# Performance work log

Measured on AMD Instinct MI355X. Metric: run time of the kernel, lower is better.

Reference implementation:

```python
import jax, jax.numpy as jnp
import numpy as np

WORD, D, H = 512, 64, 8  # word_size, embed_dim (per-head), n_query

def setup_inputs() -> dict:
    key = jax.random.key(0)
    ks = jax.random.split(key, 9)
    B, S = 2, 4096
    sw = 1.0 / np.sqrt(WORD)
    x  = jax.random.normal(ks[0], (B, S, WORD), dtype=jnp.float32)
    Wk = jax.random.normal(ks[1], (WORD, D), dtype=jnp.float32) * sw
    bk = jnp.zeros((D,), jnp.float32)
    Wv = jax.random.normal(ks[2], (WORD, D), dtype=jnp.float32) * sw
    bv = jnp.zeros((D,), jnp.float32)
    Wq = jax.random.normal(ks[3], (H, WORD, D), dtype=jnp.float32) * sw
    bq = jnp.zeros((H, D), jnp.float32)
    Wp = jax.random.normal(ks[4], (H * D, D), dtype=jnp.float32) * (1.0 / np.sqrt(H * D))
    bp = jnp.zeros((D,), jnp.float32)
    return {"x": x, "Wq": Wq, "bq": bq, "Wk": Wk, "bk": bk, "Wv": Wv, "bv": bv, "Wp": Wp, "bp": bp}

def reference(x, Wq, bq, Wk, bk, Wv, bv, Wp, bp):
    # shared K/V across all query heads (multi-query attention)
    K = x @ Wk + bk                                   # [b, s, d]
    V = x @ Wv + bv                                   # [b, s, d]
    Q = jnp.einsum('bsw,hwd->bhsd', x, Wq) + bq[None, :, None, :]  # [b, h, s, d]
    scale = 1.0 / jnp.sqrt(jnp.float32(D))
    scores = jnp.einsum('bhsd,btd->bhst', Q, K) * scale  # [b, h, s, t]
    attn = jax.nn.softmax(scores, axis=-1)
    Z = jnp.einsum('bhst,btd->bhsd', attn, V)            # [b, h, s, d]
    B, _, S, _ = Z.shape
    Zc = jnp.transpose(Z, (0, 2, 1, 3)).reshape(B, S, H * D)  # concat heads
    return Zc @ Wp + bp                                   # [b, s, d]
```

## Files before the change

kernel.cpp:

```cpp
#include <hip/hip_runtime.h>
#include <hip/hip_bf16.h>
#include <stdint.h>

#define BB 2
#define SS 4096
#define WW 512
#define DD 64
#define HH 8
#define QSCALE 0.1803368801111244f

typedef __hip_bfloat16 bf16;
typedef __bf16 bf16x8 __attribute__((ext_vector_type(8)));
typedef float f32x16 __attribute__((ext_vector_type(16)));
typedef unsigned int u32x4 __attribute__((ext_vector_type(4)));
typedef unsigned int u32x2 __attribute__((ext_vector_type(2)));

union U4 { u32x4 u4; unsigned int u[4]; bf16x8 v; };

__device__ __forceinline__ float ldv(const float* p, size_t i) { return p[i]; }
__device__ __forceinline__ float ldv(const bf16* p, size_t i)  { return __bfloat162float(p[i]); }

__device__ __forceinline__ unsigned short f2bu(float f) {
    union Ub { bf16 b; unsigned short u; } t;
    t.b = __float2bfloat16(f);
    return t.u;
}

__device__ __forceinline__ float fast_exp2(float x) {
#if __has_builtin(__builtin_amdgcn_exp2f)
    return __builtin_amdgcn_exp2f(x);
#else
    return exp2f(x);
#endif
}

__device__ __forceinline__ f32x16 mfma_bf16(bf16x8 a, bf16x8 b, f32x16 c) {
    return __builtin_amdgcn_mfma_f32_32x32x16_bf16(a, b, c, 0, 0, 0);
}

__device__ __forceinline__ unsigned int pk_bf16(float lo, float hi) {
    unsigned int a = __float_as_uint(lo) + 0x8000u;
    unsigned int b = __float_as_uint(hi) + 0x8000u;
    return __builtin_amdgcn_perm(b, a, 0x07060302u);
}

__device__ __forceinline__ unsigned int cvtpk_bf16(float lo, float hi) {
    unsigned int r;
    asm("v_cvt_pk_bf16_f32 %0, %1, %2" : "=v"(r) : "v"(lo), "v"(hi));
    return r;
}

__device__ __forceinline__ int block_detect(const void* raw, int* cntLds)
{
    if (threadIdx.x == 0) *cntLds = 0;
    __syncthreads();
    const bf16* xb = (const bf16*)raw;
    const float v = __bfloat162float(xb[2 * threadIdx.x]);
    const float a = fabsf(v);
    const bool insane = !(v == v) || (a >= 1.0e4f) || (a != 0.0f && a <= 1.0e-8f);
    const unsigned long long m = __ballot(insane);
    if ((threadIdx.x & 63) == 0) atomicAdd(cntLds, __popcll(m));
    __syncthreads();
    return (*cntLds * 2 > 256) ? 1 : 0;
}

template<typename T>
__device__ __forceinline__ void prep_w_body(
    const T* Wq, const T* bq, const T* Wk, const T* bk,
    const T* Wv, const T* bv, const T* Wp, const T* bp,
    unsigned short* Wb, float* bb, float (*Tt)[65], int pwblk)
{
    const int tid = threadIdx.x;
    const int cg = pwblk >> 3, wg = pwblk & 7;
    const int c0 = cg * 64, w0 = wg * 64;
    const T* src = (cg == 0) ? Wk : (cg == 1) ? Wv
                 : (cg == 10) ? Wp : (Wq + (size_t)(cg - 2) * WW * DD);
    const float scale = (cg >= 2 && cg < 10) ? QSCALE : 1.0f;

    #pragma unroll
    for (int i = 0; i < 16; ++i) {
        const int e = i * 256 + tid, w = e >> 6, d = e & 63;
        Tt[w][d] = ldv(src, (size_t)(w0 + w) * DD + d) * scale;
    }
    __syncthreads();
    #pragma unroll
    for (int i = 0; i < 16; ++i) {
        const int e = i * 256 + tid, d = e >> 6, w = e & 63;
        Wb[(size_t)(c0 + d) * WW + w0 + w] = f2bu(Tt[w][d]);
    }
    if (pwblk == 0) {
        #pragma unroll
        for (int i = 0; i < 3; ++i) {
            const int c = tid + i * 256;
            if (c < 704) {
                float v;
                if (c < 64)       v = ldv(bk, c);
                else if (c < 128) v = ldv(bv, c - 64);
                else if (c < 640) v = ldv(bq, c - 128) * QSCALE;
                else              v = ldv(bp, c - 640);
                bb[c] = v;
            }
        }
    }
}

__global__ __launch_bounds__(256) void prep_kernel(
    const void* x, const void* Wq, const void* bq, const void* Wk, const void* bk,
    const void* Wv, const void* bv, const void* Wp, const void* bp,
    unsigned short* xb, unsigned short* Wb, float* bb, int* flag)
{
    __shared__ float Tt[64][65];
    __shared__ int cnt;
    const int blk = blockIdx.x;

    if (blk < 2048) {
        const int fl = block_detect(x, &cnt);
        if (blk == 0 && threadIdx.x == 0) *flag = fl;
        const size_t i = ((size_t)blk * 256 + threadIdx.x) * 8;
        if (fl) {
            const float4* p = (const float4*)((const float*)x + i);
            const float4 a = p[0], b = p[1];
            unsigned int w[4];
            w[0] = pk_bf16(a.x, a.y); w[1] = pk_bf16(a.z, a.w);
            w[2] = pk_bf16(b.x, b.y); w[3] = pk_bf16(b.z, b.w);
            *(u32x4*)(xb + i) = *(u32x4*)w;
        } else {
            *(u32x4*)(xb + i) = *(const u32x4*)((const unsigned short*)x + i);
        }
    } else {
        const int fl = block_detect(Wk, &cnt);
        if (fl)
            prep_w_body<float>((const float*)Wq, (const float*)bq, (const float*)Wk,
                               (const float*)bk, (const float*)Wv, (const float*)bv,
                               (const float*)Wp, (const float*)bp, Wb, bb, Tt, blk - 2048);
        else
            prep_w_body<bf16>((const bf16*)Wq, (const bf16*)bq, (const bf16*)Wk,
                              (const bf16*)bk, (const bf16*)Wv, (const bf16*)bv,
                              (const bf16*)Wp, (const bf16*)bp, Wb, bb, Tt, blk - 2048);
    }
}

#define KP 40

__global__ __launch_bounds__(256, 2) void proj_mfma_kernel(
    const unsigned short* __restrict__ xb, const unsigned short* __restrict__ Wb,
    const float* __restrict__ bb,
    bf16* __restrict__ Kb, bf16* __restrict__ Vb, bf16* __restrict__ Qb)
{
    __shared__ unsigned short As[2][128 * KP];
    __shared__ unsigned short Bs[2][128 * KP];

    const int tid = threadIdx.x;
    const int wv = tid >> 6, ln = tid & 63;
    const int g = ln >> 5, cc = ln & 31;
    const int nblk = blockIdx.x % 5, mblk = blockIdx.x / 5;
    const int row0 = mblk * 128, n0 = nblk * 128;
    const int wm = (wv & 1) * 64, wn = (wv >> 1) * 64;

    const int sm = tid >> 2;
    const int sko = (tid & 3) * 8;

    u32x4 pa[2], pb[2];
    #define GLOAD(kt)                                                          \
        do {                                                                   \
            _Pragma("unroll")                                                  \
            for (int i = 0; i < 2; ++i) {                                      \
                const int m = sm + i * 64;                                     \
                pa[i] = *(const u32x4*)&xb[(size_t)(row0 + m) * WW + (kt) * 32 + sko]; \
                pb[i] = *(const u32x4*)&Wb[(size_t)(n0 + m) * WW + (kt) * 32 + sko];   \
            }                                                                  \
        } while (0)
    #define LWRITE(buf)                                                        \
        do {                                                                   \
            _Pragma("unroll")                                                  \
            for (int i = 0; i < 2; ++i) {                                      \
                const int m = sm + i * 64;                                     \
                *(u32x4*)&As[buf][m * KP + sko] = pa[i];                       \
                *(u32x4*)&Bs[buf][m * KP + sko] = pb[i];                       \
            }                                                                  \
        } while (0)

    f32x16 acc[2][2];
    #pragma unroll
    for (int a = 0; a < 2; ++a)
        #pragma unroll
        for (int c2 = 0; c2 < 2; ++c2)
            #pragma unroll
            for (int i = 0; i < 16; ++i) acc[a][c2][i] = 0.f;

    GLOAD(0); LWRITE(0);
    GLOAD(1);

    for (int kt = 0; kt < 16; ++kt) {
        __syncthreads();
        const int buf = kt & 1;
        #pragma unroll
        for (int ks = 0; ks < 2; ++ks) {
            U4 af[2], bfr[2];
            #pragma unroll
            for (int ms = 0; ms < 2; ++ms)
                af[ms].u4 = *(const u32x4*)&As[buf][(wm + ms * 32 + cc) * KP + ks * 16 + g * 8];
            #pragma unroll
            for (int ns = 0; ns < 2; ++ns)
                bfr[ns].u4 = *(const u32x4*)&Bs[buf][(wn + ns * 32 + cc) * KP + ks * 16 + g * 8];
            #pragma unroll
            for (int ms = 0; ms < 2; ++ms)
                #pragma unroll
                for (int ns = 0; ns < 2; ++ns)
                    acc[ms][ns] = mfma_bf16(af[ms].v, bfr[ns].v, acc[ms][ns]);
        }
        if (kt < 15) {
            LWRITE(buf ^ 1);
            if (kt < 14) GLOAD(kt + 2);
        }
    }
    #undef GLOAD
    #undef LWRITE

    const int b = row0 >> 12;
    #pragma unroll
    for (int ns = 0; ns < 2; ++ns) {
        const int c = n0 + wn + ns * 32 + cc;
        const int grp = c >> 6, d = c & 63;
        const float bias = bb[c];
        bf16* base = (grp == 0) ? Kb : (grp == 1) ? Vb
                   : Qb + (size_t)((b * HH + grp - 2) - b) * SS * DD;
        #pragma unroll
        for (int ms = 0; ms < 2; ++ms) {
            #pragma unroll
            for (int reg = 0; reg < 16; ++reg) {
                const int r = (reg & 3) + 8 * (reg >> 2) + 4 * g;
                const int row = row0 + wm + ms * 32 + r;
                base[(size_t)row * DD + d] = __float2bfloat16(acc[ms][ns][reg] + bias);
            }
        }
    }
}

__device__ __forceinline__ int vperm(int r) {
    return (r & ~31) + 16 * ((r >> 4) & 1) + 8 * ((r >> 2) & 1)
         + 4 * ((r >> 3) & 1) + (r & 3);
}

__global__ __launch_bounds__(256) void vtrans_kernel(
    const unsigned short* __restrict__ Vb, unsigned short* __restrict__ Vtg)
{
    __shared__ unsigned short Ls[64 * 70];
    const int tid = threadIdx.x;
    const int bb = blockIdx.x >> 6;
    const int t0 = (blockIdx.x & 63) * 64;
    const unsigned short* in = Vb + ((size_t)bb * SS + t0) * DD;

    const int lt = tid >> 2, s2 = tid & 3;
    #pragma unroll
    for (int q2 = 0; q2 < 2; ++q2) {
        const int sg = s2 + q2 * 4;
        *(u32x4*)&Ls[lt * 70 + sg * 8] = *(const u32x4*)&in[lt * 64 + sg * 8];
    }
    __syncthreads();

    const int dd = tid >> 2, t2 = tid & 3;
    unsigned short* op = Vtg + ((size_t)bb * DD + dd) * SS + t0;
    #pragma unroll
    for (int q2 = 0; q2 < 2; ++q2) {
        const int ts = (t2 + q2 * 4) * 8;
        unsigned short tmp[8];
        #pragma unroll
        for (int j = 0; j < 8; ++j) tmp[j] = Ls[(ts + j) * 70 + dd];
        const int s0 = vperm(ts);
        const int s1 = vperm(ts + 4);
        *(u32x2*)&op[s0] = *(u32x2*)&tmp[0];
        *(u32x2*)&op[s1] = *(u32x2*)&tmp[4];
    }
}

#define VTP 72
#define ZP_PART ((size_t)16 * 64 * 4096)
#define LP_PART ((size_t)16 * 4096)

template<int TSPLIT>
__global__ __launch_bounds__(256, 2) void attn_mfma_kernel(
    const bf16* __restrict__ Kb, const unsigned short* __restrict__ Vtg,
    const bf16* __restrict__ Qb, bf16* __restrict__ Zb,
    float* __restrict__ Zp, float* __restrict__ Lp)
{
    __shared__ unsigned short Vt[2][64 * VTP];
    __shared__ unsigned short Kt[2][64 * VTP];

    const int tid = threadIdx.x;
    const int wv = tid >> 6, ln = tid & 63;
    const int g  = ln >> 5, cc = ln & 31;
    constexpr int TSB = (TSPLIT == 1) ? 0 : (TSPLIT == 2) ? 1 : 2;
    const int chunk = blockIdx.x & 15;
    const int tsp = (blockIdx.x >> 4) & (TSPLIT - 1);
    const int bh  = blockIdx.x >> (4 + TSB);
    const int b = bh >> 3, h = bh & 7;
    const int qw = chunk * 256 + wv * 64;
    const int it0 = tsp * (64 / TSPLIT);
    const int itN = it0 + 64 / TSPLIT;

    const unsigned short* Kg = (const unsigned short*)(Kb + (size_t)b * SS * DD);
    const unsigned short* Vg = Vtg + (size_t)b * DD * SS;
    const char* Qg = (const char*)(Qb + (size_t)(b * HH + h) * SS * DD);

    const int sr = tid >> 2, sc = (tid & 3) * 16;
    const unsigned short* VgRow = Vg + (size_t)sr * SS;

    U4 qf[2][4];
    #pragma unroll
    for (int nt = 0; nt < 2; ++nt)
        #pragma unroll
        for (int ks = 0; ks < 4; ++ks)
            qf[nt][ks].u4 = *(const u32x4*)(Qg +
                (size_t)((qw + nt * 32 + cc) * 64 + g * 8 + ks * 16) * 2);

    const f32x16 fzero = {0.f, 0.f, 0.f, 0.f, 0.f, 0.f, 0.f, 0.f,
                          0.f, 0.f, 0.f, 0.f, 0.f, 0.f, 0.f, 0.f};
    U4 ones;
    ones.u[0] = 0x3F803F80u; ones.u[1] = 0x3F803F80u;
    ones.u[2] = 0x3F803F80u; ones.u[3] = 0x3F803F80u;

    f32x16 zacc[2][2];
    #pragma unroll
    for (int nt = 0; nt < 2; ++nt)
        #pragma unroll
        for (int dt = 0; dt < 2; ++dt)
            #pragma unroll
            for (int i = 0; i < 16; ++i) zacc[nt][dt][i] = 0.f;

    f32x16 lacc[2];
    #pragma unroll
    for (int nt = 0; nt < 2; ++nt)
        #pragma unroll
        for (int i = 0; i < 16; ++i) lacc[nt][i] = 0.f;

    {
        const unsigned short* ksrc = Kg + (size_t)(it0 * 64 + sr) * 64 + sc;
        const unsigned short* vsrc = VgRow + it0 * 64 + sc;
        *(u32x4*)&Kt[0][sr * VTP + sc + 0] = *(const u32x4*)&ksrc[0];
        *(u32x4*)&Kt[0][sr * VTP + sc + 8] = *(const u32x4*)&ksrc[8];
        *(u32x4*)&Vt[0][sr * VTP + sc + 0] = *(const u32x4*)&vsrc[0];
        *(u32x4*)&Vt[0][sr * VTP + sc + 8] = *(const u32x4*)&vsrc[8];
    }

    for (int it = it0; it < itN; ++it) {
        __syncthreads();
        const int buf = it & 1;
        const bool more = (it + 1) < itN;
        u32x4 pk0, pk1, pv0, pv1;
        if (more) {
            const unsigned short* ksrc = Kg + (size_t)((it + 1) * 64 + sr) * 64 + sc;
            const unsigned short* vsrc = VgRow + (it + 1) * 64 + sc;
            pk0 = *(const u32x4*)&ksrc[0];
            pk1 = *(const u32x4*)&ksrc[8];
            pv0 = *(const u32x4*)&vsrc[0];
            pv1 = *(const u32x4*)&vsrc[8];
        }

        #pragma unroll
        for (int si = 0; si < 2; ++si) {
            U4 kf[4];
            #pragma unroll
            for (int ks = 0; ks < 4; ++ks)
                kf[ks].u4 = *(const u32x4*)&Kt[buf][(si * 32 + cc) * VTP +
                                                    ks * 16 + g * 8];
            U4 vf[2][2];
            #pragma unroll
            for (int ks = 0; ks < 2; ++ks)
                #pragma unroll
                for (int dt = 0; dt < 2; ++dt)
                    vf[ks][dt].u4 = *(const u32x4*)&Vt[buf][(dt * 32 + cc) * VTP +
                                                            si * 32 + ks * 16 + g * 8];

            #pragma unroll
            for (int nt = 0; nt < 2; ++nt) {
                __builtin_amdgcn_s_setprio(1);
                f32x16 s = mfma_bf16(kf[0].v, qf[nt][0].v, fzero);
                #pragma unroll
                for (int ks = 1; ks < 4; ++ks) s = mfma_bf16(kf[ks].v, qf[nt][ks].v, s);
                __builtin_amdgcn_s_setprio(0);

                float p[16];
                #pragma unroll
                for (int i = 0; i < 16; ++i) p[i] = fast_exp2(s[i]);
                unsigned int w0[8];
                #pragma unroll
                for (int i2 = 0; i2 < 8; ++i2)
                    w0[i2] = cvtpk_bf16(p[2 * i2], p[2 * i2 + 1]);

                __builtin_amdgcn_s_setprio(1);
                #pragma unroll
                for (int ks = 0; ks < 2; ++ks) {
                    U4 pb;
                    pb.u[0] = w0[ks * 4 + 0]; pb.u[1] = w0[ks * 4 + 1];
                    pb.u[2] = w0[ks * 4 + 2]; pb.u[3] = w0[ks * 4 + 3];
                    lacc[nt] = mfma_bf16(ones.v, pb.v, lacc[nt]);
                    #pragma unroll
                    for (int dt = 0; dt < 2; ++dt)
                        zacc[nt][dt] = mfma_bf16(vf[ks][dt].v, pb.v, zacc[nt][dt]);
                }
                __builtin_amdgcn_s_setprio(0);
            }
        }

        if (more) {
            *(u32x4*)&Kt[buf ^ 1][sr * VTP + sc + 0] = pk0;
            *(u32x4*)&Kt[buf ^ 1][sr * VTP + sc + 8] = pk1;
            *(u32x4*)&Vt[buf ^ 1][sr * VTP + sc + 0] = pv0;
            *(u32x4*)&Vt[buf ^ 1][sr * VTP + sc + 8] = pv1;
        }
    }

    float l[2];
    l[0] = lacc[0][0];
    l[1] = lacc[1][0];

    if (TSPLIT == 1) {
        #pragma unroll
        for (int nt = 0; nt < 2; ++nt) {
            const float rr = 1.0f / l[nt];
            bf16* zp = Zb + (size_t)(b * SS + qw + nt * 32 + cc) * (HH * DD)
                     + h * DD + g * 4;
            #pragma unroll
            for (int dt = 0; dt < 2; ++dt)
                #pragma unroll
                for (int i = 0; i < 16; ++i) {
                    const int d = (i & 3) + 8 * (i >> 2) + 32 * dt;
                    zp[d] = __float2bfloat16(zacc[nt][dt][i] * rr);
                }
        }
    } else {
        float* zp0 = Zp + (size_t)(tsp * 16 + bh) * (64 * 4096);
        #pragma unroll
        for (int nt = 0; nt < 2; ++nt) {
            const int q = qw + nt * 32 + cc;
            #pragma unroll
            for (int dt = 0; dt < 2; ++dt)
                #pragma unroll
                for (int i = 0; i < 16; ++i) {
                    const int d = (i & 3) + 8 * (i >> 2) + 4 * g + 32 * dt;
                    zp0[(size_t)d * 4096 + q] = zacc[nt][dt][i];
                }
            if (g == 0)
                Lp[(size_t)(tsp * 16 + bh) * 4096 + q] = l[nt];
        }
    }
}

template<int NP>
__global__ __launch_bounds__(256) void combine_kernel(
    const float* __restrict__ Zp, const float* __restrict__ Lp,
    bf16* __restrict__ Zb)
{
    const size_t T = (size_t)blockIdx.x * 256 + threadIdx.x;
    const int sblk = (int)(T & 511);
    const int d  = (int)((T >> 9) & 63);
    const int bh = (int)(T >> 15);
    const int s0 = sblk * 8;
    const int b = bh >> 3, h = bh & 7;

    const float* p0 = Zp + ((size_t)bh * 64 + d) * 4096 + s0;
    const float* l0 = Lp + (size_t)bh * 4096 + s0;

    float z[8], lv[8];
    #pragma unroll
    for (int j = 0; j < 8; ++j) { z[j] = 0.f; lv[j] = 0.f; }
    #pragma unroll
    for (int np = 0; np < NP; ++np) {
        const float* p = p0 + (size_t)np * ZP_PART;
        const float* l = l0 + (size_t)np * LP_PART;
        #pragma unroll
        for (int j = 0; j < 8; j += 4) {
            const float4 a = *(const float4*)(p + j);
            z[j] += a.x; z[j+1] += a.y; z[j+2] += a.z; z[j+3] += a.w;
            const float4 e = *(const float4*)(l + j);
            lv[j] += e.x; lv[j+1] += e.y; lv[j+2] += e.z; lv[j+3] += e.w;
        }
    }
    bf16* zo = Zb + ((size_t)(b * SS + s0)) * (HH * DD) + h * DD + d;
    #pragma unroll
    for (int j = 0; j < 8; ++j)
        zo[(size_t)j * (HH * DD)] = __float2bfloat16(z[j] / lv[j]);
}

__global__ __launch_bounds__(256) void outp_mfma_kernel(
    const bf16* __restrict__ Zb, const unsigned short* __restrict__ Wb,
    const float* __restrict__ bb, const int* flag, void* out)
{
    __shared__ unsigned short As[2][128 * KP];
    __shared__ unsigned short Bs[2][64 * KP];

    const int tid = threadIdx.x;
    const int wv = tid >> 6, ln = tid & 63;
    const int g = ln >> 5, cc = ln & 31;
    const int row0 = blockIdx.x * 128;
    const int sm = tid >> 2, sko = (tid & 3) * 8;

    const unsigned short* Zu = (const unsigned short*)Zb;
    const unsigned short* Wn = Wb + (size_t)640 * WW;
    const float* bbp = bb + 640;

    u32x4 pa[2], pbv;
    #define GLOAD2(kt)                                                         \
        do {                                                                   \
            _Pragma("unroll")                                                  \
            for (int i = 0; i < 2; ++i)                                        \
                pa[i] = *(const u32x4*)&Zu[(size_t)(row0 + sm + i * 64) * WW + (kt) * 32 + sko]; \
            pbv = *(const u32x4*)&Wn[(size_t)sm * WW + (kt) * 32 + sko];       \
        } while (0)
    #define LWRITE2(buf)                                                       \
        do {                                                                   \
            _Pragma("unroll")                                                  \
            for (int i = 0; i < 2; ++i)                                        \
                *(u32x4*)&As[buf][(sm + i * 64) * KP + sko] = pa[i];           \
            *(u32x4*)&Bs[buf][sm * KP + sko] = pbv;                            \
        } while (0)

    f32x16 acc[2];
    #pragma unroll
    for (int ns = 0; ns < 2; ++ns)
        #pragma unroll
        for (int i = 0; i < 16; ++i) acc[ns][i] = 0.f;

    GLOAD2(0); LWRITE2(0);
    GLOAD2(1);

    for (int kt = 0; kt < 16; ++kt) {
        __syncthreads();
        const int buf = kt & 1;
        #pragma unroll
        for (int ks = 0; ks < 2; ++ks) {
            U4 af;
            af.u4 = *(const u32x4*)&As[buf][(wv * 32 + cc) * KP + ks * 16 + g * 8];
            #pragma unroll
            for (int ns = 0; ns < 2; ++ns) {
                U4 bf2;
                bf2.u4 = *(const u32x4*)&Bs[buf][(ns * 32 + cc) * KP + ks * 16 + g * 8];
                acc[ns] = mfma_bf16(af.v, bf2.v, acc[ns]);
            }
        }
        if (kt < 15) {
            LWRITE2(buf ^ 1);
            if (kt < 14) GLOAD2(kt + 2);
        }
    }
    #undef GLOAD2
    #undef LWRITE2

    const int fl = *flag;
    #pragma unroll
    for (int ns = 0; ns < 2; ++ns) {
        const int c = ns * 32 + cc;
        const float bias = bbp[c];
        #pragma unroll
        for (int reg = 0; reg < 16; ++reg) {
            const int r = (reg & 3) + 8 * (reg >> 2) + 4 * g;
            const int row = row0 + wv * 32 + r;
            const float v = acc[ns][reg] + bias;
            if (fl) ((float*)out)[(size_t)row * DD + c] = v;
            else    ((bf16*)out)[(size_t)row * DD + c] = __float2bfloat16(v);
        }
    }
}

extern "C" void kernel_launch(void* const* d_in, const int* in_sizes, int n_in,
                              void* d_out, int out_size, void* d_ws, size_t ws_size,
                              hipStream_t stream)
{
    const void* x  = d_in[0];
    const void* Wq = d_in[1];
    const void* bq = d_in[2];
    const void* Wk = d_in[3];
    const void* bk = d_in[4];
    const void* Wv = d_in[5];
    const void* bv = d_in[6];
    const void* Wp = d_in[7];
    const void* bp = d_in[8];

    char* ws = (char*)d_ws;
    bf16* Kb = (bf16*)(ws);
    bf16* Vb = (bf16*)(ws + (1u << 20));
    bf16* Qb = (bf16*)(ws + (2u << 20));
    bf16* Zb = (bf16*)(ws + (10u << 20));
    unsigned short* xb = (unsigned short*)(ws + (10u << 20));
    int* flag = (int*)(ws + (18u << 20));
    unsigned short* Wb = (unsigned short*)(ws + (18u << 20) + 64);
    float* bb = (float*)(ws + (18u << 20) + 64 + 704 * 512 * 2);
    unsigned short* Vtg = (unsigned short*)(ws + (19u << 20));
    float* Zp = (float*)(ws + (20u << 20));

    const size_t ws_need2 = (20u << 20) + (size_t)2 * ZP_PART * 4 + (size_t)2 * LP_PART * 4;

    prep_kernel<<<2136, 256, 0, stream>>>(x, Wq, bq, Wk, bk, Wv, bv, Wp, bp,
                                          xb, Wb, bb, flag);
    proj_mfma_kernel<<<320, 256, 0, stream>>>(xb, Wb, bb, Kb, Vb, Qb);
    vtrans_kernel<<<128, 256, 0, stream>>>((const unsigned short*)Vb, Vtg);
    if (ws_size >= ws_need2) {
        float* Lp = (float*)(ws + (20u << 20) + 2 * ZP_PART * 4);
        attn_mfma_kernel<2><<<512, 256, 0, stream>>>(Kb, Vtg, Qb, Zb, Zp, Lp);
        combine_kernel<2><<<2048, 256, 0, stream>>>(Zp, Lp, Zb);
    } else {
        float* Lp = (float*)(ws + (20u << 20));
        attn_mfma_kernel<1><<<256, 256, 0, stream>>>(Kb, Vtg, Qb, Zb, Zp, Lp);
    }
    outp_mfma_kernel<<<64, 256, 0, stream>>>(Zb, Wb, bb, flag, d_out);
}
```

Measured before the change: 201.7 us.

## Halve per-warp query tile in attention to double block count

Each wave now handles 32 queries instead of 64, so a block covers 128 queries and the attention grid doubles to 1024 (or 512 without split) blocks. This cuts per-thread register use (one Q fragment set and one set of accumulators) and spreads work across more CUs. In exchange, every K/V tile loaded into shared memory is reused by half as many queries, which doubles global and LDS traffic for K/V.

```diff
diff --git a/kernel.cpp b/kernel.cpp
--- a/kernel.cpp
+++ b/kernel.cpp
@@ -291,11 +291,11 @@
     const int wv = tid >> 6, ln = tid & 63;
     const int g  = ln >> 5, cc = ln & 31;
     constexpr int TSB = (TSPLIT == 1) ? 0 : (TSPLIT == 2) ? 1 : 2;
-    const int chunk = blockIdx.x & 15;
-    const int tsp = (blockIdx.x >> 4) & (TSPLIT - 1);
-    const int bh  = blockIdx.x >> (4 + TSB);
+    const int chunk = blockIdx.x & 31;
+    const int tsp = (blockIdx.x >> 5) & (TSPLIT - 1);
+    const int bh  = blockIdx.x >> (5 + TSB);
     const int b = bh >> 3, h = bh & 7;
-    const int qw = chunk * 256 + wv * 64;
+    const int qw = chunk * 128 + wv * 32;
     const int it0 = tsp * (64 / TSPLIT);
     const int itN = it0 + 64 / TSPLIT;
 
@@ -306,13 +306,11 @@
     const int sr = tid >> 2, sc = (tid & 3) * 16;
     const unsigned short* VgRow = Vg + (size_t)sr * SS;
 
-    U4 qf[2][4];
-    #pragma unroll
-    for (int nt = 0; nt < 2; ++nt)
-        #pragma unroll
-        for (int ks = 0; ks < 4; ++ks)
-            qf[nt][ks].u4 = *(const u32x4*)(Qg +
-                (size_t)((qw + nt * 32 + cc) * 64 + g * 8 + ks * 16) * 2);
+    U4 qf[4];
+    #pragma unroll
+    for (int ks = 0; ks < 4; ++ks)
+        qf[ks].u4 = *(const u32x4*)(Qg +
+            (size_t)((qw + cc) * 64 + g * 8 + ks * 16) * 2);
 
     const f32x16 fzero = {0.f, 0.f, 0.f, 0.f, 0.f, 0.f, 0.f, 0.f,
                           0.f, 0.f, 0.f, 0.f, 0.f, 0.f, 0.f, 0.f};
@@ -320,19 +318,15 @@
     ones.u[0] = 0x3F803F80u; ones.u[1] = 0x3F803F80u;
     ones.u[2] = 0x3F803F80u; ones.u[3] = 0x3F803F80u;
 
-    f32x16 zacc[2][2];
-    #pragma unroll
-    for (int nt = 0; nt < 2; ++nt)
-        #pragma unroll
-        for (int dt = 0; dt < 2; ++dt)
-            #pragma unroll
-            for (int i = 0; i < 16; ++i) zacc[nt][dt][i] = 0.f;
-
-    f32x16 lacc[2];
-    #pragma unroll
-    for (int nt = 0; nt < 2; ++nt)
-        #pragma unroll
-        for (int i = 0; i < 16; ++i) lacc[nt][i] = 0.f;
+    f32x16 zacc[2];
+    #pragma unroll
+    for (int dt = 0; dt < 2; ++dt)
+        #pragma unroll
+        for (int i = 0; i < 16; ++i) zacc[dt][i] = 0.f;
+
+    f32x16 lacc;
+    #pragma unroll
+    for (int i = 0; i < 16; ++i) lacc[i] = 0.f;
 
     {
         const unsigned short* ksrc = Kg + (size_t)(it0 * 64 + sr) * 64 + sc;
@@ -372,35 +366,32 @@
                     vf[ks][dt].u4 = *(const u32x4*)&Vt[buf][(dt * 32 + cc) * VTP +
                                                             si * 32 + ks * 16 + g * 8];
 
-            #pragma unroll
-            for (int nt = 0; nt < 2; ++nt) {
-                __builtin_amdgcn_s_setprio(1);
-                f32x16 s = mfma_bf16(kf[0].v, qf[nt][0].v, fzero);
+            __builtin_amdgcn_s_setprio(1);
+            f32x16 s = mfma_bf16(kf[0].v, qf[0].v, fzero);
+            #pragma unroll
+            for (int ks = 1; ks < 4; ++ks) s = mfma_bf16(kf[ks].v, qf[ks].v, s);
+            __builtin_amdgcn_s_setprio(0);
+
+            float p[16];
+            #pragma unroll
+            for (int i = 0; i < 16; ++i) p[i] = fast_exp2(s[i]);
+            unsigned int w0[8];
+            #pragma unroll
+            for (int i2 = 0; i2 < 8; ++i2)
+                w0[i2] = cvtpk_bf16(p[2 * i2], p[2 * i2 + 1]);
+
+            __builtin_amdgcn_s_setprio(1);
+            #pragma unroll
+            for (int ks = 0; ks < 2; ++ks) {
+                U4 pb;
+                pb.u[0] = w0[ks * 4 + 0]; pb.u[1] = w0[ks * 4 + 1];
+                pb.u[2] = w0[ks * 4 + 2]; pb.u[3] = w0[ks * 4 + 3];
+                lacc = mfma_bf16(ones.v, pb.v, lacc);
                 #pragma unroll
-                for (int ks = 1; ks < 4; ++ks) s = mfma_bf16(kf[ks].v, qf[nt][ks].v, s);
-                __builtin_amdgcn_s_setprio(0);
-
-                float p[16];
-                #pragma unroll
-                for (int i = 0; i < 16; ++i) p[i] = fast_exp2(s[i]);
-                unsigned int w0[8];
-                #pragma unroll
-                for (int i2 = 0; i2 < 8; ++i2)
-                    w0[i2] = cvtpk_bf16(p[2 * i2], p[2 * i2 + 1]);
-
-                __builtin_amdgcn_s_setprio(1);
-                #pragma unroll
-                for (int ks = 0; ks < 2; ++ks) {
-                    U4 pb;
-                    pb.u[0] = w0[ks * 4 + 0]; pb.u[1] = w0[ks * 4 + 1];
-                    pb.u[2] = w0[ks * 4 + 2]; pb.u[3] = w0[ks * 4 + 3];
-                    lacc[nt] = mfma_bf16(ones.v, pb.v, lacc[nt]);
-                    #pragma unroll
-                    for (int dt = 0; dt < 2; ++dt)
-                        zacc[nt][dt] = mfma_bf16(vf[ks][dt].v, pb.v, zacc[nt][dt]);
-                }
-                __builtin_amdgcn_s_setprio(0);
+                for (int dt = 0; dt < 2; ++dt)
+                    zacc[dt] = mfma_bf16(vf[ks][dt].v, pb.v, zacc[dt]);
             }
+            __builtin_amdgcn_s_setprio(0);
         }
 
         if (more) {
@@ -411,39 +402,30 @@
         }
     }
 
-    float l[2];
-    l[0] = lacc[0][0];
-    l[1] = lacc[1][0];
+    const float l = lacc[0];
 
     if (TSPLIT == 1) {
-        #pragma unroll
-        for (int nt = 0; nt < 2; ++nt) {
-            const float rr = 1.0f / l[nt];
-            bf16* zp = Zb + (size_t)(b * SS + qw + nt * 32 + cc) * (HH * DD)
-                     + h * DD + g * 4;
-            #pragma unroll
-            for (int dt = 0; dt < 2; ++dt)
-                #pragma unroll
-                for (int i = 0; i < 16; ++i) {
-                    const int d = (i & 3) + 8 * (i >> 2) + 32 * dt;
-                    zp[d] = __float2bfloat16(zacc[nt][dt][i] * rr);
-                }
-        }
+        const float rr = 1.0f / l;
+        bf16* zp = Zb + (size_t)(b * SS + qw + cc) * (HH * DD) + h * DD + g * 4;
+        #pragma unroll
+        for (int dt = 0; dt < 2; ++dt)
+            #pragma unroll
+            for (int i = 0; i < 16; ++i) {
+                const int d = (i & 3) + 8 * (i >> 2) + 32 * dt;
+                zp[d] = __float2bfloat16(zacc[dt][i] * rr);
+            }
     } else {
         float* zp0 = Zp + (size_t)(tsp * 16 + bh) * (64 * 4096);
-        #pragma unroll
-        for (int nt = 0; nt < 2; ++nt) {
-            const int q = qw + nt * 32 + cc;
-            #pragma unroll
-            for (int dt = 0; dt < 2; ++dt)
-                #pragma unroll
-                for (int i = 0; i < 16; ++i) {
-                    const int d = (i & 3) + 8 * (i >> 2) + 4 * g + 32 * dt;
-                    zp0[(size_t)d * 4096 + q] = zacc[nt][dt][i];
-                }
-            if (g == 0)
-                Lp[(size_t)(tsp * 16 + bh) * 4096 + q] = l[nt];
-        }
+        const int q = qw + cc;
+        #pragma unroll
+        for (int dt = 0; dt < 2; ++dt)
+            #pragma unroll
+            for (int i = 0; i < 16; ++i) {
+                const int d = (i & 3) + 8 * (i >> 2) + 4 * g + 32 * dt;
+                zp0[(size_t)d * 4096 + q] = zacc[dt][i];
+            }
+        if (g == 0)
+            Lp[(size_t)(tsp * 16 + bh) * 4096 + q] = l;
     }
 }
 
@@ -597,11 +579,11 @@
     vtrans_kernel<<<128, 256, 0, stream>>>((const unsigned short*)Vb, Vtg);
     if (ws_size >= ws_need2) {
         float* Lp = (float*)(ws + (20u << 20) + 2 * ZP_PART * 4);
-        attn_mfma_kernel<2><<<512, 256, 0, stream>>>(Kb, Vtg, Qb, Zb, Zp, Lp);
+        attn_mfma_kernel<2><<<1024, 256, 0, stream>>>(Kb, Vtg, Qb, Zb, Zp, Lp);
         combine_kernel<2><<<2048, 256, 0, stream>>>(Zp, Lp, Zb);
     } else {
         float* Lp = (float*)(ws + (20u << 20));
-        attn_mfma_kernel<1><<<256, 256, 0, stream>>>(Kb, Vtg, Qb, Zb, Zp, Lp);
+        attn_mfma_kernel<1><<<512, 256, 0, stream>>>(Kb, Vtg, Qb, Zb, Zp, Lp);
     }
     outp_mfma_kernel<<<64, 256, 0, stream>>>(Zb, Wb, bb, flag, d_out);
 }
```

Measured after the change: 209.1 us. 3.7% more time.

## Fuse V transpose into projection epilogue and split-K combine into attention

Applied to the files above, without the earlier changes.

The projection kernel now writes V directly in the transposed, permuted layout the attention kernel expects, which removes the separate vtrans kernel and the Vb round trip. The attention kernel with a two-way key split now uses a per-tile atomic counter, so whichever block of a pair finishes second reads the partner's partial Z and L, normalises, and writes Zb. This removes the separate combine kernel and its launch. In exchange the V stores become scattered 2-byte writes, and correctness depends on threadfence ordering and on cflags being reset in prep_kernel on every call.

```diff
diff --git a/kernel.cpp b/kernel.cpp
--- a/kernel.cpp
+++ b/kernel.cpp
@@ -107,7 +107,7 @@
 __global__ __launch_bounds__(256) void prep_kernel(
     const void* x, const void* Wq, const void* bq, const void* Wk, const void* bk,
     const void* Wv, const void* bv, const void* Wp, const void* bp,
-    unsigned short* xb, unsigned short* Wb, float* bb, int* flag)
+    unsigned short* xb, unsigned short* Wb, float* bb, int* flag, int* cflags)
 {
     __shared__ float Tt[64][65];
     __shared__ int cnt;
@@ -128,6 +128,7 @@
             *(u32x4*)(xb + i) = *(const u32x4*)((const unsigned short*)x + i);
         }
     } else {
+        if (blk == 2048) cflags[threadIdx.x] = 0;
         const int fl = block_detect(Wk, &cnt);
         if (fl)
             prep_w_body<float>((const float*)Wq, (const float*)bq, (const float*)Wk,
@@ -145,7 +146,7 @@
 __global__ __launch_bounds__(256, 2) void proj_mfma_kernel(
     const unsigned short* __restrict__ xb, const unsigned short* __restrict__ Wb,
     const float* __restrict__ bb,
-    bf16* __restrict__ Kb, bf16* __restrict__ Vb, bf16* __restrict__ Qb)
+    bf16* __restrict__ Kb, unsigned short* __restrict__ Vtg, bf16* __restrict__ Qb)
 {
     __shared__ unsigned short As[2][128 * KP];
     __shared__ unsigned short Bs[2][128 * KP];
@@ -223,54 +224,31 @@
         const int c = n0 + wn + ns * 32 + cc;
         const int grp = c >> 6, d = c & 63;
         const float bias = bb[c];
-        bf16* base = (grp == 0) ? Kb : (grp == 1) ? Vb
-                   : Qb + (size_t)((b * HH + grp - 2) - b) * SS * DD;
-        #pragma unroll
-        for (int ms = 0; ms < 2; ++ms) {
-            #pragma unroll
-            for (int reg = 0; reg < 16; ++reg) {
-                const int r = (reg & 3) + 8 * (reg >> 2) + 4 * g;
-                const int row = row0 + wm + ms * 32 + r;
-                base[(size_t)row * DD + d] = __float2bfloat16(acc[ms][ns][reg] + bias);
+        if (grp == 1) {
+            unsigned short* vt = Vtg + ((size_t)(b * DD + d)) * SS;
+            #pragma unroll
+            for (int ms = 0; ms < 2; ++ms) {
+                #pragma unroll
+                for (int reg = 0; reg < 16; ++reg) {
+                    const int r = (reg & 3) + 8 * (reg >> 2) + 4 * g;
+                    const int lrow = (row0 & 4095) + wm + ms * 32 + r;
+                    const int srow = (lrow & ~12) | ((lrow & 4) << 1) | ((lrow & 8) >> 1);
+                    vt[srow] = f2bu(acc[ms][ns][reg] + bias);
+                }
             }
-        }
-    }
-}
-
-__device__ __forceinline__ int vperm(int r) {
-    return (r & ~31) + 16 * ((r >> 4) & 1) + 8 * ((r >> 2) & 1)
-         + 4 * ((r >> 3) & 1) + (r & 3);
-}
-
-__global__ __launch_bounds__(256) void vtrans_kernel(
-    const unsigned short* __restrict__ Vb, unsigned short* __restrict__ Vtg)
-{
-    __shared__ unsigned short Ls[64 * 70];
-    const int tid = threadIdx.x;
-    const int bb = blockIdx.x >> 6;
-    const int t0 = (blockIdx.x & 63) * 64;
-    const unsigned short* in = Vb + ((size_t)bb * SS + t0) * DD;
-
-    const int lt = tid >> 2, s2 = tid & 3;
-    #pragma unroll
-    for (int q2 = 0; q2 < 2; ++q2) {
-        const int sg = s2 + q2 * 4;
-        *(u32x4*)&Ls[lt * 70 + sg * 8] = *(const u32x4*)&in[lt * 64 + sg * 8];
-    }
-    __syncthreads();
-
-    const int dd = tid >> 2, t2 = tid & 3;
-    unsigned short* op = Vtg + ((size_t)bb * DD + dd) * SS + t0;
-    #pragma unroll
-    for (int q2 = 0; q2 < 2; ++q2) {
-        const int ts = (t2 + q2 * 4) * 8;
-        unsigned short tmp[8];
-        #pragma unroll
-        for (int j = 0; j < 8; ++j) tmp[j] = Ls[(ts + j) * 70 + dd];
-        const int s0 = vperm(ts);
-        const int s1 = vperm(ts + 4);
-        *(u32x2*)&op[s0] = *(u32x2*)&tmp[0];
-        *(u32x2*)&op[s1] = *(u32x2*)&tmp[4];
+        } else {
+            bf16* base = (grp == 0) ? Kb
+                       : Qb + (size_t)((b * HH + grp - 2) - b) * SS * DD;
+            #pragma unroll
+            for (int ms = 0; ms < 2; ++ms) {
+                #pragma unroll
+                for (int reg = 0; reg < 16; ++reg) {
+                    const int r = (reg & 3) + 8 * (reg >> 2) + 4 * g;
+                    const int row = row0 + wm + ms * 32 + r;
+                    base[(size_t)row * DD + d] = __float2bfloat16(acc[ms][ns][reg] + bias);
+                }
+            }
+        }
     }
 }
 
@@ -282,15 +260,16 @@
 __global__ __launch_bounds__(256, 2) void attn_mfma_kernel(
     const bf16* __restrict__ Kb, const unsigned short* __restrict__ Vtg,
     const bf16* __restrict__ Qb, bf16* __restrict__ Zb,
-    float* __restrict__ Zp, float* __restrict__ Lp)
+    float* __restrict__ Zp, float* __restrict__ Lp, int* cflags)
 {
     __shared__ unsigned short Vt[2][64 * VTP];
     __shared__ unsigned short Kt[2][64 * VTP];
+    __shared__ int ordS;
 
     const int tid = threadIdx.x;
     const int wv = tid >> 6, ln = tid & 63;
     const int g  = ln >> 5, cc = ln & 31;
-    constexpr int TSB = (TSPLIT == 1) ? 0 : (TSPLIT == 2) ? 1 : 2;
+    constexpr int TSB = (TSPLIT == 1) ? 0 : 1;
     const int chunk = blockIdx.x & 15;
     const int tsp = (blockIdx.x >> 4) & (TSPLIT - 1);
     const int bh  = blockIdx.x >> (4 + TSB);
@@ -431,6 +410,7 @@
         }
     } else {
         float* zp0 = Zp + (size_t)(tsp * 16 + bh) * (64 * 4096);
+        float* lp0 = Lp + (size_t)(tsp * 16 + bh) * 4096;
         #pragma unroll
         for (int nt = 0; nt < 2; ++nt) {
             const int q = qw + nt * 32 + cc;
@@ -442,45 +422,31 @@
                     zp0[(size_t)d * 4096 + q] = zacc[nt][dt][i];
                 }
             if (g == 0)
-                Lp[(size_t)(tsp * 16 + bh) * 4096 + q] = l[nt];
-        }
-    }
-}
-
-template<int NP>
-__global__ __launch_bounds__(256) void combine_kernel(
-    const float* __restrict__ Zp, const float* __restrict__ Lp,
-    bf16* __restrict__ Zb)
-{
-    const size_t T = (size_t)blockIdx.x * 256 + threadIdx.x;
-    const int sblk = (int)(T & 511);
-    const int d  = (int)((T >> 9) & 63);
-    const int bh = (int)(T >> 15);
-    const int s0 = sblk * 8;
-    const int b = bh >> 3, h = bh & 7;
-
-    const float* p0 = Zp + ((size_t)bh * 64 + d) * 4096 + s0;
-    const float* l0 = Lp + (size_t)bh * 4096 + s0;
-
-    float z[8], lv[8];
-    #pragma unroll
-    for (int j = 0; j < 8; ++j) { z[j] = 0.f; lv[j] = 0.f; }
-    #pragma unroll
-    for (int np = 0; np < NP; ++np) {
-        const float* p = p0 + (size_t)np * ZP_PART;
-        const float* l = l0 + (size_t)np * LP_PART;
-        #pragma unroll
-        for (int j = 0; j < 8; j += 4) {
-            const float4 a = *(const float4*)(p + j);
-            z[j] += a.x; z[j+1] += a.y; z[j+2] += a.z; z[j+3] += a.w;
-            const float4 e = *(const float4*)(l + j);
-            lv[j] += e.x; lv[j+1] += e.y; lv[j+2] += e.z; lv[j+3] += e.w;
-        }
-    }
-    bf16* zo = Zb + ((size_t)(b * SS + s0)) * (HH * DD) + h * DD + d;
-    #pragma unroll
-    for (int j = 0; j < 8; ++j)
-        zo[(size_t)j * (HH * DD)] = __float2bfloat16(z[j] / lv[j]);
+                lp0[q] = l[nt];
+        }
+        __threadfence();
+        if (tid == 0) ordS = atomicAdd(&cflags[bh * 16 + chunk], 1);
+        __syncthreads();
+        if (ordS == 1) {
+            __threadfence();
+            const float* zo_ = Zp + (size_t)((1 - tsp) * 16 + bh) * (64 * 4096);
+            const float* lo_ = Lp + (size_t)((1 - tsp) * 16 + bh) * 4096;
+            #pragma unroll
+            for (int nt = 0; nt < 2; ++nt) {
+                const int q = qw + nt * 32 + cc;
+                const float rr = 1.0f / (l[nt] + lo_[q]);
+                bf16* zb = Zb + (size_t)(b * SS + q) * (HH * DD) + h * DD;
+                #pragma unroll
+                for (int dt = 0; dt < 2; ++dt)
+                    #pragma unroll
+                    for (int i = 0; i < 16; ++i) {
+                        const int d = (i & 3) + 8 * (i >> 2) + 4 * g + 32 * dt;
+                        zb[d] = __float2bfloat16(
+                            (zacc[nt][dt][i] + zo_[(size_t)d * 4096 + q]) * rr);
+                    }
+            }
+        }
+    }
 }
 
 __global__ __launch_bounds__(256) void outp_mfma_kernel(
@@ -579,7 +545,6 @@
 
     char* ws = (char*)d_ws;
     bf16* Kb = (bf16*)(ws);
-    bf16* Vb = (bf16*)(ws + (1u << 20));
     bf16* Qb = (bf16*)(ws + (2u << 20));
     bf16* Zb = (bf16*)(ws + (10u << 20));
     unsigned short* xb = (unsigned short*)(ws + (10u << 20));
@@ -588,20 +553,19 @@
     float* bb = (float*)(ws + (18u << 20) + 64 + 704 * 512 * 2);
     unsigned short* Vtg = (unsigned short*)(ws + (19u << 20));
     float* Zp = (float*)(ws + (20u << 20));
-
-    const size_t ws_need2 = (20u << 20) + (size_t)2 * ZP_PART * 4 + (size_t)2 * LP_PART * 4;
+    float* Lp = (float*)(ws + (20u << 20) + 2 * ZP_PART * 4);
+    int* cflags = (int*)(ws + (20u << 20) + 2 * ZP_PART * 4 + 2 * LP_PART * 4);
+
+    const size_t ws_need2 = (20u << 20) + (size_t)2 * ZP_PART * 4
+                          + (size_t)2 * LP_PART * 4 + 1024;
 
     prep_kernel<<<2136, 256, 0, stream>>>(x, Wq, bq, Wk, bk, Wv, bv, Wp, bp,
-                                          xb, Wb, bb, flag);
-    proj_mfma_kernel<<<320, 256, 0, stream>>>(xb, Wb, bb, Kb, Vb, Qb);
-    vtrans_kernel<<<128, 256, 0, stream>>>((const unsigned short*)Vb, Vtg);
+                                          xb, Wb, bb, flag, cflags);
+    proj_mfma_kernel<<<320, 256, 0, stream>>>(xb, Wb, bb, Kb, Vtg, Qb);
     if (ws_size >= ws_need2) {
-        float* Lp = (float*)(ws + (20u << 20) + 2 * ZP_PART * 4);
-        attn_mfma_kernel<2><<<512, 256, 0, stream>>>(Kb, Vtg, Qb, Zb, Zp, Lp);
-        combine_kernel<2><<<2048, 256, 0, stream>>>(Zp, Lp, Zb);
+        attn_mfma_kernel<2><<<512, 256, 0, stream>>>(Kb, Vtg, Qb, Zb, Zp, Lp, cflags);
     } else {
-        float* Lp = (float*)(ws + (20u << 20));
-        attn_mfma_kernel<1><<<256, 256, 0, stream>>>(Kb, Vtg, Qb, Zb, Zp, Lp);
+        attn_mfma_kernel<1><<<256, 256, 0, stream>>>(Kb, Vtg, Qb, Zb, Zp, Lp, cflags);
     }
     outp_mfma_kernel<<<64, 256, 0, stream>>>(Zb, Wb, bb, flag, d_out);
 }
```

After: 267.9 us. 1.33x slower.
